# Performance work log

Hardware: AMD Instinct MI355X
Metric: run time of the kernel (lower is better)

## Reference

```python
import jax, jax.numpy as jnp
import numpy as np

N = 100000
E = 800000
D = 128
OUT = 128


def setup_inputs() -> dict:
    key = jax.random.key(0)
    k = jax.random.split(key, 6)
    x = jax.random.normal(k[0], (N, D), dtype=jnp.float32)
    edge_index = jax.random.randint(k[1], (2, E), 0, N, dtype=jnp.int64)
    # Linear params stored as [in, out] so forward is x @ W + b
    Wl = jax.random.normal(k[2], (D, OUT), dtype=jnp.float32) / np.sqrt(D)
    bl = jax.random.normal(k[3], (OUT,), dtype=jnp.float32) * 0.01
    Wr = jax.random.normal(k[4], (D, OUT), dtype=jnp.float32) / np.sqrt(D)
    br = jax.random.normal(k[5], (OUT,), dtype=jnp.float32) * 0.01
    return {"x": x, "edge_index": edge_index, "Wl": Wl, "bl": bl, "Wr": Wr, "br": br}


def reference(x, edge_index, Wl, bl, Wr, br):
    n = x.shape[0]
    tgt = edge_index[0]   # node receiving the aggregation (edge_index[0] == i)
    nbr = edge_index[1]   # neighbor whose features are gathered
    # scatter-mean: sum neighbor features per target node, divide by degree
    agg_sum = jax.ops.segment_sum(x[nbr], tgt, num_segments=n)          # [N, D]
    deg = jax.ops.segment_sum(jnp.ones((edge_index.shape[1],), x.dtype), tgt, num_segments=n)
    agg = agg_sum / jnp.maximum(deg, 1.0)[:, None]  # zero rows stay zero (no neighbors)
    out = jax.nn.relu(x @ Wl + bl + agg @ Wr + br)
    norm = jnp.linalg.norm(out, axis=1, keepdims=True) + 1e-6
    return out / norm
```

## Files before the change

### kernel.cpp

```cpp
#include <hip/hip_runtime.h>

#define D 128
#define BM 64

typedef __attribute__((ext_vector_type(8))) short bf16x8;
typedef __attribute__((ext_vector_type(4))) float f32x4;

__device__ __forceinline__ float bf2f(unsigned short u) {
    union { unsigned int i; float f; } v; v.i = ((unsigned int)u) << 16; return v.f;
}
__device__ __forceinline__ unsigned short f2bf(float f) {
    union { float f; unsigned int i; } v; v.f = f;
    unsigned int x = v.i;
    unsigned int r = (x + 0x7fffu + ((x >> 16) & 1u)) >> 16;
    return (unsigned short)r;
}

__global__ __launch_bounds__(256) void gs_prep(
    const float* __restrict__ x, const float* __restrict__ Wl,
    const float* __restrict__ Wr, const int* __restrict__ ei,
    unsigned short* __restrict__ x_bf, unsigned short* __restrict__ Bp,
    int* __restrict__ counts, int* __restrict__ flag, int n, int E) {
    const int tid0 = blockIdx.x * 256 + threadIdx.x;
    const int stride = gridDim.x * 256;

    if (blockIdx.x == 0 && threadIdx.x < 64) {
        int lim = (E < 64) ? E : 64;
        int odd = (threadIdx.x < lim) ? ei[2 * threadIdx.x + 1] : 0;
        unsigned long long b = __ballot(odd != 0);
        if (threadIdx.x == 0) *flag = (b != 0ULL) ? 1 : 0;
    }
    for (int i = tid0; i < 2 * n; i += stride) counts[i] = 0;
    const int nch = n * (D / 8);
    for (int i = tid0; i < nch; i += stride) {
        const float4 a = *(const float4*)(x + (size_t)i * 8);
        const float4 b = *(const float4*)(x + (size_t)i * 8 + 4);
        unsigned short o[8] = {f2bf(a.x), f2bf(a.y), f2bf(a.z), f2bf(a.w),
                               f2bf(b.x), f2bf(b.y), f2bf(b.z), f2bf(b.w)};
        *(uint4*)(x_bf + (size_t)i * 8) = *(const uint4*)o;
    }
    for (int q = tid0; q < 4096; q += stride) {
        int g = q & 3, c = (q >> 2) & 127, s = q >> 9;
        unsigned short o[8];
#pragma unroll
        for (int j = 0; j < 8; ++j) {
            int k = s * 32 + g * 8 + j;
            float w = (k < 128) ? Wl[k * 128 + c] : Wr[(k - 128) * 128 + c];
            o[j] = f2bf(w);
        }
        *(uint4*)(Bp + (size_t)q * 8) = *(const uint4*)o;
    }
}

__global__ void gs_hist(const int* __restrict__ ei, int* __restrict__ counts,
                        const int* __restrict__ flag, int E, int n) {
    int e = blockIdx.x * blockDim.x + threadIdx.x;
    if (e >= E) return;
    int tgt = (*flag) ? ei[e] : ei[2 * e];
    if ((unsigned)tgt < (unsigned)n) atomicAdd(&counts[tgt], 1);
}

__global__ __launch_bounds__(256) void gs_scanA(const int* __restrict__ counts,
                                                int* __restrict__ offs,
                                                int* __restrict__ partials, int n) {
    __shared__ int s[256];
    const int tid = threadIdx.x;
    const int i = blockIdx.x * 256 + tid;
    int v = (i < n) ? counts[i] : 0;
    s[tid] = v;
    __syncthreads();
    for (int off = 1; off < 256; off <<= 1) {
        int t = (tid >= off) ? s[tid - off] : 0;
        __syncthreads();
        s[tid] += t;
        __syncthreads();
    }
    if (i < n) offs[i] = s[tid] - v;
    if (tid == 255) partials[blockIdx.x] = s[255];
}

__global__ __launch_bounds__(512) void gs_scanB(int* __restrict__ partials, int nb) {
    __shared__ int s[512];
    const int tid = threadIdx.x;
    int v = (tid < nb) ? partials[tid] : 0;
    s[tid] = v;
    __syncthreads();
    for (int off = 1; off < 512; off <<= 1) {
        int t = (tid >= off) ? s[tid - off] : 0;
        __syncthreads();
        s[tid] += t;
        __syncthreads();
    }
    if (tid < nb) partials[tid] = s[tid] - v;
}

__global__ void gs_bin(const int* __restrict__ ei, const int* __restrict__ offs,
                       const int* __restrict__ partials, int* __restrict__ cursor,
                       int* __restrict__ sorted_nbr, const int* __restrict__ flag,
                       int E, int n) {
    int e = blockIdx.x * blockDim.x + threadIdx.x;
    if (e >= E) return;
    int tgt, nbr;
    if (*flag) { tgt = ei[e];     nbr = ei[E + e]; }
    else       { tgt = ei[2 * e]; nbr = ei[2 * (E + e)]; }
    if ((unsigned)tgt >= (unsigned)n || (unsigned)nbr >= (unsigned)n) return;
    int p = offs[tgt] + partials[tgt >> 8] + atomicAdd(&cursor[tgt], 1);
    sorted_nbr[p] = nbr;
}

__global__ __launch_bounds__(256) void gs_agg(
    const int* __restrict__ sorted_nbr, const int* __restrict__ counts,
    const int* __restrict__ offs, const int* __restrict__ partials,
    const unsigned short* __restrict__ x_bf, unsigned short* __restrict__ agg_bf,
    int n) {
    int node = blockIdx.x * 4 + (threadIdx.x >> 6);
    if (node >= n) return;
    const int lane = threadIdx.x & 63;
    const int qw = lane >> 4, c = lane & 15;
    const int cnt = counts[node];
    const int start = offs[node] + partials[node >> 8];
    float a[8] = {};
    for (int j = 0; j < cnt; j += 4) {
        int jj = j + qw;
        if (jj < cnt) {
            int nbr = sorted_nbr[start + jj];
            uint4 raw = *(const uint4*)(x_bf + (size_t)nbr * D + c * 8);
            const unsigned short* u = (const unsigned short*)&raw;
#pragma unroll
            for (int e = 0; e < 8; ++e) a[e] += bf2f(u[e]);
        }
    }
#pragma unroll
    for (int e = 0; e < 8; ++e) {
        a[e] += __shfl_xor(a[e], 16, 64);
        a[e] += __shfl_xor(a[e], 32, 64);
    }
    if (qw == 0) {
        const float inv = (cnt > 0) ? (1.0f / (float)cnt) : 0.0f;
        unsigned short o[8];
#pragma unroll
        for (int e = 0; e < 8; ++e) o[e] = f2bf(a[e] * inv);
        *(uint4*)(agg_bf + (size_t)node * D + c * 8) = *(const uint4*)o;
    }
}

__global__ __launch_bounds__(256) void gs_fused(
    const unsigned short* __restrict__ x_bf, const unsigned short* __restrict__ agg_bf,
    const unsigned short* __restrict__ Bp,
    const float* __restrict__ bl, const float* __restrict__ br,
    float* __restrict__ out, int n) {
    __shared__ unsigned short sA[BM][256];

    const int tid = threadIdx.x;
    const int wave = tid >> 6, lane = tid & 63;
    const int g = lane >> 4, c = lane & 15;
    const int r0 = blockIdx.x * BM;

#pragma unroll
    for (int it = 0; it < 8; ++it) {
        int idx = it * 256 + tid;
        int row = idx >> 5, ch = idx & 31;
        int grow = r0 + row;
        uint4 val = make_uint4(0u, 0u, 0u, 0u);
        if (grow < n) {
            const unsigned short* src = (ch < 16)
                ? (x_bf + (size_t)grow * D + ch * 8)
                : (agg_bf + (size_t)grow * D + (ch - 16) * 8);
            val = *(const uint4*)src;
        }
        int sch = ch ^ (row & 7);
        *(uint4*)((char*)&sA[0][0] + row * 512 + sch * 16) = val;
    }
    __syncthreads();

    f32x4 acc[8] = {};
    const int arow = wave * 16 + c;
    const int axor = (arow & 7);
#pragma unroll
    for (int s = 0; s < 8; ++s) {
        bf16x8 afrag = *(const bf16x8*)((const char*)&sA[0][0] +
                                        arow * 512 + (((s * 4 + g) ^ axor) * 16));
#pragma unroll
        for (int f = 0; f < 8; ++f) {
            bf16x8 bfrag = *(const bf16x8*)(Bp + (size_t)(((s * 128 + f * 16 + c) * 4 + g) * 8));
            acc[f] = __builtin_amdgcn_mfma_f32_16x16x32_bf16(afrag, bfrag, acc[f], 0, 0, 0);
        }
    }

    float v[8][4];
    float sumsq[4] = {0.f, 0.f, 0.f, 0.f};
#pragma unroll
    for (int f = 0; f < 8; ++f) {
        float bb = bl[f * 16 + c] + br[f * 16 + c];
#pragma unroll
        for (int r = 0; r < 4; ++r) {
            float y = fmaxf(acc[f][r] + bb, 0.f);
            v[f][r] = y;
            sumsq[r] += y * y;
        }
    }
#pragma unroll
    for (int r = 0; r < 4; ++r) {
        float s = sumsq[r];
        s += __shfl_xor(s, 1, 64);
        s += __shfl_xor(s, 2, 64);
        s += __shfl_xor(s, 4, 64);
        s += __shfl_xor(s, 8, 64);
        sumsq[r] = 1.0f / (sqrtf(s) + 1e-6f);
    }
    const int baserow = r0 + wave * 16 + g * 4;
#pragma unroll
    for (int r = 0; r < 4; ++r) {
        int row = baserow + r;
        if (row < n) {
#pragma unroll
            for (int f = 0; f < 8; ++f)
                out[(size_t)row * D + f * 16 + c] = v[f][r] * sumsq[r];
        }
    }
}

extern "C" void kernel_launch(void* const* d_in, const int* in_sizes, int n_in,
                              void* d_out, int out_size, void* d_ws, size_t ws_size,
                              hipStream_t stream) {
    const float* x  = (const float*)d_in[0];
    const int*   ei = (const int*)d_in[1];
    const float* Wl = (const float*)d_in[2];
    const float* bl = (const float*)d_in[3];
    const float* Wr = (const float*)d_in[4];
    const float* br = (const float*)d_in[5];
    float* out = (float*)d_out;

    const int n = in_sizes[0] / D;
    const int E = in_sizes[1] / 2;
    const int nb = (n + 255) / 256;

    unsigned short* x_bf   = (unsigned short*)d_ws;
    unsigned short* agg_bf = x_bf + (size_t)n * D;
    unsigned short* Bp     = agg_bf + (size_t)n * D;
    int*   counts   = (int*)(Bp + 32768);
    int*   cursor   = counts + n;
    int*   flag     = cursor + n;
    int*   offs     = flag + 4;
    int*   partials = offs + n;
    int*   sorted   = partials + 512;

    gs_prep<<<4096, 256, 0, stream>>>(x, Wl, Wr, ei, x_bf, Bp, counts, flag, n, E);
    gs_hist<<<(E + 255) / 256, 256, 0, stream>>>(ei, counts, flag, E, n);
    gs_scanA<<<nb, 256, 0, stream>>>(counts, offs, partials, n);
    gs_scanB<<<1, 512, 0, stream>>>(partials, nb);
    gs_bin<<<(E + 255) / 256, 256, 0, stream>>>(ei, offs, partials, cursor, sorted, flag, E, n);
    gs_agg<<<(n + 3) / 4, 256, 0, stream>>>(sorted, counts, offs, partials, x_bf, agg_bf, n);
    gs_fused<<<(n + BM - 1) / BM, 256, 0, stream>>>(x_bf, agg_bf, Bp, bl, br, out, n);
}
```

Baseline: 267.8 us.

## Fuse neighbor aggregation into GEMM kernel and merge histogram into prep

Moves the mean-aggregation gather into the fused MFMA kernel so each block writes aggregated rows straight into shared memory, removing the agg_bf round trip through global memory and one launch. Folds the degree histogram into the prep kernel, which also writes compacted 32-bit tgt/nbr arrays so the bin kernel reads less edge data. Zeroing of counts moves to a separate small kernel. The risk is that the gather now runs inside the GEMM blocks one node at a time per wave, which may lower memory-level parallelism and occupancy for the latency-bound gather.

```diff
diff --git a/kernel.cpp b/kernel.cpp
--- a/kernel.cpp
+++ b/kernel.cpp
@@ -16,21 +16,39 @@
     return (unsigned short)r;
 }
 
+__global__ void gs_zero_i(int* __restrict__ p, int n) {
+    int i = blockIdx.x * blockDim.x + threadIdx.x;
+    int st = gridDim.x * blockDim.x;
+    for (; i < n; i += st) p[i] = 0;
+}
+
 __global__ __launch_bounds__(256) void gs_prep(
     const float* __restrict__ x, const float* __restrict__ Wl,
     const float* __restrict__ Wr, const int* __restrict__ ei,
     unsigned short* __restrict__ x_bf, unsigned short* __restrict__ Bp,
-    int* __restrict__ counts, int* __restrict__ flag, int n, int E) {
-    const int tid0 = blockIdx.x * 256 + threadIdx.x;
-    const int stride = gridDim.x * 256;
-
-    if (blockIdx.x == 0 && threadIdx.x < 64) {
+    int* __restrict__ tgt32, int* __restrict__ nbr32,
+    int* __restrict__ counts, int n, int E) {
+    __shared__ int sflag;
+    if (threadIdx.x < 64) {
         int lim = (E < 64) ? E : 64;
         int odd = (threadIdx.x < lim) ? ei[2 * threadIdx.x + 1] : 0;
         unsigned long long b = __ballot(odd != 0);
-        if (threadIdx.x == 0) *flag = (b != 0ULL) ? 1 : 0;
-    }
-    for (int i = tid0; i < 2 * n; i += stride) counts[i] = 0;
+        if (threadIdx.x == 0) sflag = (b != 0ULL) ? 1 : 0;
+    }
+    __syncthreads();
+    const int is32 = sflag;
+    const int tid0 = blockIdx.x * 256 + threadIdx.x;
+    const int stride = gridDim.x * 256;
+
+    for (int e = tid0; e < E; e += stride) {
+        int tgt, nbr;
+        if (is32) { tgt = ei[e];     nbr = ei[E + e]; }
+        else      { tgt = ei[2 * e]; nbr = ei[2 * (E + e)]; }
+        int ok = ((unsigned)tgt < (unsigned)n) && ((unsigned)nbr < (unsigned)n);
+        tgt32[e] = ok ? tgt : -1;
+        nbr32[e] = nbr;
+        if (ok) atomicAdd(&counts[tgt], 1);
+    }
     const int nch = n * (D / 8);
     for (int i = tid0; i < nch; i += stride) {
         const float4 a = *(const float4*)(x + (size_t)i * 8);
@@ -50,14 +68,6 @@
         }
         *(uint4*)(Bp + (size_t)q * 8) = *(const uint4*)o;
     }
-}
-
-__global__ void gs_hist(const int* __restrict__ ei, int* __restrict__ counts,
-                        const int* __restrict__ flag, int E, int n) {
-    int e = blockIdx.x * blockDim.x + threadIdx.x;
-    if (e >= E) return;
-    int tgt = (*flag) ? ei[e] : ei[2 * e];
-    if ((unsigned)tgt < (unsigned)n) atomicAdd(&counts[tgt], 1);
 }
 
 __global__ __launch_bounds__(256) void gs_scanA(const int* __restrict__ counts,
@@ -94,86 +104,79 @@
     if (tid < nb) partials[tid] = s[tid] - v;
 }
 
-__global__ void gs_bin(const int* __restrict__ ei, const int* __restrict__ offs,
-                       const int* __restrict__ partials, int* __restrict__ cursor,
-                       int* __restrict__ sorted_nbr, const int* __restrict__ flag,
-                       int E, int n) {
+__global__ void gs_bin(const int* __restrict__ tgt32, const int* __restrict__ nbr32,
+                       const int* __restrict__ offs, const int* __restrict__ partials,
+                       int* __restrict__ cursor, int* __restrict__ sorted_nbr, int E) {
     int e = blockIdx.x * blockDim.x + threadIdx.x;
     if (e >= E) return;
-    int tgt, nbr;
-    if (*flag) { tgt = ei[e];     nbr = ei[E + e]; }
-    else       { tgt = ei[2 * e]; nbr = ei[2 * (E + e)]; }
-    if ((unsigned)tgt >= (unsigned)n || (unsigned)nbr >= (unsigned)n) return;
+    int tgt = tgt32[e];
+    if (tgt < 0) return;
     int p = offs[tgt] + partials[tgt >> 8] + atomicAdd(&cursor[tgt], 1);
-    sorted_nbr[p] = nbr;
-}
-
-__global__ __launch_bounds__(256) void gs_agg(
-    const int* __restrict__ sorted_nbr, const int* __restrict__ counts,
-    const int* __restrict__ offs, const int* __restrict__ partials,
-    const unsigned short* __restrict__ x_bf, unsigned short* __restrict__ agg_bf,
-    int n) {
-    int node = blockIdx.x * 4 + (threadIdx.x >> 6);
-    if (node >= n) return;
-    const int lane = threadIdx.x & 63;
-    const int qw = lane >> 4, c = lane & 15;
-    const int cnt = counts[node];
-    const int start = offs[node] + partials[node >> 8];
-    float a[8] = {};
-    for (int j = 0; j < cnt; j += 4) {
-        int jj = j + qw;
-        if (jj < cnt) {
-            int nbr = sorted_nbr[start + jj];
-            uint4 raw = *(const uint4*)(x_bf + (size_t)nbr * D + c * 8);
-            const unsigned short* u = (const unsigned short*)&raw;
-#pragma unroll
-            for (int e = 0; e < 8; ++e) a[e] += bf2f(u[e]);
-        }
-    }
-#pragma unroll
-    for (int e = 0; e < 8; ++e) {
-        a[e] += __shfl_xor(a[e], 16, 64);
-        a[e] += __shfl_xor(a[e], 32, 64);
-    }
-    if (qw == 0) {
-        const float inv = (cnt > 0) ? (1.0f / (float)cnt) : 0.0f;
-        unsigned short o[8];
-#pragma unroll
-        for (int e = 0; e < 8; ++e) o[e] = f2bf(a[e] * inv);
-        *(uint4*)(agg_bf + (size_t)node * D + c * 8) = *(const uint4*)o;
-    }
+    sorted_nbr[p] = nbr32[e];
 }
 
 __global__ __launch_bounds__(256) void gs_fused(
-    const unsigned short* __restrict__ x_bf, const unsigned short* __restrict__ agg_bf,
-    const unsigned short* __restrict__ Bp,
+    const unsigned short* __restrict__ x_bf, const int* __restrict__ sorted_nbr,
+    const int* __restrict__ counts, const int* __restrict__ offs,
+    const int* __restrict__ partials, const unsigned short* __restrict__ Bp,
     const float* __restrict__ bl, const float* __restrict__ br,
     float* __restrict__ out, int n) {
     __shared__ unsigned short sA[BM][256];
 
     const int tid = threadIdx.x;
     const int wave = tid >> 6, lane = tid & 63;
-    const int g = lane >> 4, c = lane & 15;
+    const int qw = lane >> 4, c = lane & 15;
     const int r0 = blockIdx.x * BM;
 
 #pragma unroll
-    for (int it = 0; it < 8; ++it) {
+    for (int it = 0; it < 4; ++it) {
         int idx = it * 256 + tid;
-        int row = idx >> 5, ch = idx & 31;
+        int row = idx >> 4, ch = idx & 15;
         int grow = r0 + row;
         uint4 val = make_uint4(0u, 0u, 0u, 0u);
-        if (grow < n) {
-            const unsigned short* src = (ch < 16)
-                ? (x_bf + (size_t)grow * D + ch * 8)
-                : (agg_bf + (size_t)grow * D + (ch - 16) * 8);
-            val = *(const uint4*)src;
-        }
+        if (grow < n) val = *(const uint4*)(x_bf + (size_t)grow * D + ch * 8);
         int sch = ch ^ (row & 7);
         *(uint4*)((char*)&sA[0][0] + row * 512 + sch * 16) = val;
     }
+
+    {
+        int myn = r0 + wave * 16 + c;
+        int cnt_l = 0, start_l = 0;
+        if (lane < 16 && myn < n) {
+            cnt_l = counts[myn];
+            start_l = offs[myn] + partials[myn >> 8];
+        }
+        for (int i = 0; i < 16; ++i) {
+            const int cnt = __shfl(cnt_l, i, 64);
+            const int start = __shfl(start_l, i, 64);
+            float a[8] = {};
+            for (int j = qw; j < cnt; j += 4) {
+                int nbr = sorted_nbr[start + j];
+                uint4 raw = *(const uint4*)(x_bf + (size_t)nbr * D + c * 8);
+                const unsigned short* u = (const unsigned short*)&raw;
+#pragma unroll
+                for (int e = 0; e < 8; ++e) a[e] += bf2f(u[e]);
+            }
+#pragma unroll
+            for (int e = 0; e < 8; ++e) {
+                a[e] += __shfl_xor(a[e], 16, 64);
+                a[e] += __shfl_xor(a[e], 32, 64);
+            }
+            if (qw == 0) {
+                const float inv = (cnt > 0) ? (1.0f / (float)cnt) : 0.0f;
+                unsigned short o[8];
+#pragma unroll
+                for (int e = 0; e < 8; ++e) o[e] = f2bf(a[e] * inv);
+                int row = wave * 16 + i;
+                int sch = (16 + c) ^ (row & 7);
+                *(uint4*)((char*)&sA[0][0] + row * 512 + sch * 16) = *(const uint4*)o;
+            }
+        }
+    }
     __syncthreads();
 
     f32x4 acc[8] = {};
+    const int g = qw;
     const int arow = wave * 16 + c;
     const int axor = (arow & 7);
 #pragma unroll
@@ -235,21 +238,20 @@
     const int E = in_sizes[1] / 2;
     const int nb = (n + 255) / 256;
 
-    unsigned short* x_bf   = (unsigned short*)d_ws;
-    unsigned short* agg_bf = x_bf + (size_t)n * D;
-    unsigned short* Bp     = agg_bf + (size_t)n * D;
-    int*   counts   = (int*)(Bp + 32768);
-    int*   cursor   = counts + n;
-    int*   flag     = cursor + n;
-    int*   offs     = flag + 4;
-    int*   partials = offs + n;
-    int*   sorted   = partials + 512;
-
-    gs_prep<<<4096, 256, 0, stream>>>(x, Wl, Wr, ei, x_bf, Bp, counts, flag, n, E);
-    gs_hist<<<(E + 255) / 256, 256, 0, stream>>>(ei, counts, flag, E, n);
+    unsigned short* x_bf = (unsigned short*)d_ws;
+    unsigned short* Bp   = x_bf + (size_t)n * D;
+    int* counts   = (int*)(Bp + 32768);
+    int* cursor   = counts + n;
+    int* offs     = cursor + n;
+    int* partials = offs + n;
+    int* tgt32    = partials + 512;
+    int* nbr32    = tgt32 + E;
+    int* sorted   = nbr32 + E;
+
+    gs_zero_i<<<512, 256, 0, stream>>>(counts, 2 * n);
+    gs_prep<<<4096, 256, 0, stream>>>(x, Wl, Wr, ei, x_bf, Bp, tgt32, nbr32, counts, n, E);
     gs_scanA<<<nb, 256, 0, stream>>>(counts, offs, partials, n);
     gs_scanB<<<1, 512, 0, stream>>>(partials, nb);
-    gs_bin<<<(E + 255) / 256, 256, 0, stream>>>(ei, offs, partials, cursor, sorted, flag, E, n);
-    gs_agg<<<(n + 3) / 4, 256, 0, stream>>>(sorted, counts, offs, partials, x_bf, agg_bf, n);
-    gs_fused<<<(n + BM - 1) / BM, 256, 0, stream>>>(x_bf, agg_bf, Bp, bl, br, out, n);
-}
+    gs_bin<<<(E + 255) / 256, 256, 0, stream>>>(tgt32, nbr32, offs, partials, cursor, sorted, E);
+    gs_fused<<<(n + BM - 1) / BM, 256, 0, stream>>>(x_bf, sorted, counts, offs, partials, Bp, bl, br, out, n);
+}
```

Result: slower. 280.8 us (+4.8%).

## Fold histogram into prep, record atomic rank to skip second atomic pass

Applied to the files above, without the earlier changes.

The histogram pass moves into the prep kernel. The rank returned by each counts atomicAdd is packed together with the target index into a per-edge word, so the binning kernel places each edge without a second atomic cursor pass. Counts are zeroed with a memset, the separate hist kernel and cursor array are removed, and the aggregation loop is unrolled by two to keep more gathers in flight. The cost is an extra 4-byte-per-edge buffer, and the packing assumes node ids fit in 18 bits and ranks in 14 bits.

```diff
diff --git a/kernel.cpp b/kernel.cpp
--- a/kernel.cpp
+++ b/kernel.cpp
@@ -20,17 +20,32 @@
     const float* __restrict__ x, const float* __restrict__ Wl,
     const float* __restrict__ Wr, const int* __restrict__ ei,
     unsigned short* __restrict__ x_bf, unsigned short* __restrict__ Bp,
-    int* __restrict__ counts, int* __restrict__ flag, int n, int E) {
-    const int tid0 = blockIdx.x * 256 + threadIdx.x;
-    const int stride = gridDim.x * 256;
-
-    if (blockIdx.x == 0 && threadIdx.x < 64) {
+    unsigned int* __restrict__ packed, int* __restrict__ counts,
+    int* __restrict__ flag, int n, int E) {
+    __shared__ int sflag;
+    if (threadIdx.x < 64) {
         int lim = (E < 64) ? E : 64;
         int odd = (threadIdx.x < lim) ? ei[2 * threadIdx.x + 1] : 0;
         unsigned long long b = __ballot(odd != 0);
-        if (threadIdx.x == 0) *flag = (b != 0ULL) ? 1 : 0;
-    }
-    for (int i = tid0; i < 2 * n; i += stride) counts[i] = 0;
+        if (threadIdx.x == 0) {
+            sflag = (b != 0ULL) ? 1 : 0;
+            if (blockIdx.x == 0) *flag = sflag;
+        }
+    }
+    __syncthreads();
+    const int is32 = sflag;
+    const int tid0 = blockIdx.x * 256 + threadIdx.x;
+    const int stride = gridDim.x * 256;
+
+    for (int e = tid0; e < E; e += stride) {
+        int tgt = is32 ? ei[e] : ei[2 * e];
+        if ((unsigned)tgt < (unsigned)n) {
+            unsigned int rank = (unsigned int)atomicAdd(&counts[tgt], 1);
+            packed[e] = (rank << 18) | (unsigned int)tgt;
+        } else {
+            packed[e] = 0xFFFFFFFFu;
+        }
+    }
     const int nch = n * (D / 8);
     for (int i = tid0; i < nch; i += stride) {
         const float4 a = *(const float4*)(x + (size_t)i * 8);
@@ -50,14 +65,6 @@
         }
         *(uint4*)(Bp + (size_t)q * 8) = *(const uint4*)o;
     }
-}
-
-__global__ void gs_hist(const int* __restrict__ ei, int* __restrict__ counts,
-                        const int* __restrict__ flag, int E, int n) {
-    int e = blockIdx.x * blockDim.x + threadIdx.x;
-    if (e >= E) return;
-    int tgt = (*flag) ? ei[e] : ei[2 * e];
-    if ((unsigned)tgt < (unsigned)n) atomicAdd(&counts[tgt], 1);
 }
 
 __global__ __launch_bounds__(256) void gs_scanA(const int* __restrict__ counts,
@@ -94,17 +101,19 @@
     if (tid < nb) partials[tid] = s[tid] - v;
 }
 
-__global__ void gs_bin(const int* __restrict__ ei, const int* __restrict__ offs,
-                       const int* __restrict__ partials, int* __restrict__ cursor,
+__global__ void gs_bin(const unsigned int* __restrict__ packed,
+                       const int* __restrict__ ei,
+                       const int* __restrict__ offs, const int* __restrict__ partials,
                        int* __restrict__ sorted_nbr, const int* __restrict__ flag,
                        int E, int n) {
     int e = blockIdx.x * blockDim.x + threadIdx.x;
     if (e >= E) return;
-    int tgt, nbr;
-    if (*flag) { tgt = ei[e];     nbr = ei[E + e]; }
-    else       { tgt = ei[2 * e]; nbr = ei[2 * (E + e)]; }
-    if ((unsigned)tgt >= (unsigned)n || (unsigned)nbr >= (unsigned)n) return;
-    int p = offs[tgt] + partials[tgt >> 8] + atomicAdd(&cursor[tgt], 1);
+    unsigned int v = packed[e];
+    unsigned int tgt = v & 0x3FFFFu;
+    if (tgt >= (unsigned)n) return;
+    int nbr = (*flag) ? ei[E + e] : ei[2 * (E + e)];
+    if ((unsigned)nbr >= (unsigned)n) return;
+    int p = offs[tgt] + partials[tgt >> 8] + (int)(v >> 18);
     sorted_nbr[p] = nbr;
 }
 
@@ -120,15 +129,25 @@
     const int cnt = counts[node];
     const int start = offs[node] + partials[node >> 8];
     float a[8] = {};
-    for (int j = 0; j < cnt; j += 4) {
-        int jj = j + qw;
-        if (jj < cnt) {
-            int nbr = sorted_nbr[start + jj];
-            uint4 raw = *(const uint4*)(x_bf + (size_t)nbr * D + c * 8);
-            const unsigned short* u = (const unsigned short*)&raw;
-#pragma unroll
-            for (int e = 0; e < 8; ++e) a[e] += bf2f(u[e]);
-        }
+    int j = qw;
+    for (; j + 4 < cnt; j += 8) {
+        int n1 = sorted_nbr[start + j];
+        int n2 = sorted_nbr[start + j + 4];
+        uint4 r1 = *(const uint4*)(x_bf + (size_t)n1 * D + c * 8);
+        uint4 r2 = *(const uint4*)(x_bf + (size_t)n2 * D + c * 8);
+        const unsigned short* u1 = (const unsigned short*)&r1;
+        const unsigned short* u2 = (const unsigned short*)&r2;
+#pragma unroll
+        for (int e = 0; e < 8; ++e) a[e] += bf2f(u1[e]);
+#pragma unroll
+        for (int e = 0; e < 8; ++e) a[e] += bf2f(u2[e]);
+    }
+    if (j < cnt) {
+        int n1 = sorted_nbr[start + j];
+        uint4 r1 = *(const uint4*)(x_bf + (size_t)n1 * D + c * 8);
+        const unsigned short* u1 = (const unsigned short*)&r1;
+#pragma unroll
+        for (int e = 0; e < 8; ++e) a[e] += bf2f(u1[e]);
     }
 #pragma unroll
     for (int e = 0; e < 8; ++e) {
@@ -238,18 +257,18 @@
     unsigned short* x_bf   = (unsigned short*)d_ws;
     unsigned short* agg_bf = x_bf + (size_t)n * D;
     unsigned short* Bp     = agg_bf + (size_t)n * D;
-    int*   counts   = (int*)(Bp + 32768);
-    int*   cursor   = counts + n;
-    int*   flag     = cursor + n;
-    int*   offs     = flag + 4;
-    int*   partials = offs + n;
-    int*   sorted   = partials + 512;
-
-    gs_prep<<<4096, 256, 0, stream>>>(x, Wl, Wr, ei, x_bf, Bp, counts, flag, n, E);
-    gs_hist<<<(E + 255) / 256, 256, 0, stream>>>(ei, counts, flag, E, n);
+    int* counts   = (int*)(Bp + 32768);
+    int* offs     = counts + n;
+    int* partials = offs + n;
+    int* flag     = partials + 512;
+    unsigned int* packed = (unsigned int*)(flag + 4);
+    int* sorted   = (int*)(packed + E);
+
+    hipMemsetAsync(counts, 0, (size_t)n * sizeof(int), stream);
+    gs_prep<<<4096, 256, 0, stream>>>(x, Wl, Wr, ei, x_bf, Bp, packed, counts, flag, n, E);
     gs_scanA<<<nb, 256, 0, stream>>>(counts, offs, partials, n);
     gs_scanB<<<1, 512, 0, stream>>>(partials, nb);
-    gs_bin<<<(E + 255) / 256, 256, 0, stream>>>(ei, offs, partials, cursor, sorted, flag, E, n);
+    gs_bin<<<(E + 255) / 256, 256, 0, stream>>>(packed, ei, offs, partials, sorted, flag, E, n);
     gs_agg<<<(n + 3) / 4, 256, 0, stream>>>(sorted, counts, offs, partials, x_bf, agg_bf, n);
     gs_fused<<<(n + BM - 1) / BM, 256, 0, stream>>>(x_bf, agg_bf, Bp, bl, br, out, n);
 }
```

Result: faster. 225.4 us (-15.8%).
